# Optimization experiments

Hardware: AMD Instinct MI355X
Metric: run time of the kernel (lower is better)

Reference implementation:

```python
import jax, jax.numpy as jnp
import numpy as np

N_NODES = 50000
N_GRAPHS = 2048
BN_EPS = 1e-5


def setup_inputs() -> dict:
    key = jax.random.key(0)
    ks = jax.random.split(key, 12)
    n_feat, dim, n_out, n_edges = 128, 128, 12, 800000
    x = jax.random.normal(ks[0], (N_NODES, n_feat), dtype=jnp.float32)
    edge_index = jax.random.randint(ks[1], (2, n_edges), 0, N_NODES, dtype=jnp.int32)
    batch = jnp.sort(jax.random.randint(ks[2], (N_NODES,), 0, N_GRAPHS, dtype=jnp.int32))
    def lin(k, fan_in, fan_out):
        bound = 1.0 / np.sqrt(fan_in)
        kw, kb = jax.random.split(k)
        W = jax.random.uniform(kw, (fan_in, fan_out), minval=-bound, maxval=bound, dtype=jnp.float32)
        b = jax.random.uniform(kb, (fan_out,), minval=-bound, maxval=bound, dtype=jnp.float32)
        return W, b
    W1, b1 = lin(ks[3], n_feat, dim)
    W2, b2 = lin(ks[4], dim, dim)
    gamma = jnp.ones((dim,), dtype=jnp.float32)
    beta = jnp.zeros((dim,), dtype=jnp.float32)
    Wf1, bf1 = lin(ks[5], dim, 2 * dim)
    Wf2, bf2 = lin(ks[6], 2 * dim, n_out)
    return {"x": x, "edge_index": edge_index, "batch": batch,
            "W1": W1, "b1": b1, "W2": W2, "b2": b2,
            "gamma": gamma, "beta": beta,
            "Wf1": Wf1, "bf1": bf1, "Wf2": Wf2, "bf2": bf2}


def reference(x, edge_index, batch, W1, b1, W2, b2, gamma, beta, Wf1, bf1, Wf2, bf2):
    src, dst = edge_index[0], edge_index[1]
    # GINConv (eps=0): h = nn1(x + sum_{j in N(i)} x_j), scatter-add at dst
    agg = jax.ops.segment_sum(x[src], dst, num_segments=N_NODES)  # [N, F]
    h = x + agg
    h = jax.nn.relu(h @ W1 + b1) @ W2 + b2  # nn1 MLP
    h = jax.nn.relu(h)
    # BatchNorm1d (training mode: batch statistics, biased variance)
    mean = jnp.mean(h, axis=0)
    var = jnp.mean((h - mean) ** 2, axis=0)
    h = (h - mean) * jax.lax.rsqrt(var + BN_EPS) * gamma + beta
    # global_add_pool over graphs
    g = jax.ops.segment_sum(h, batch, num_segments=N_GRAPHS)  # [G, dim]
    g = jax.nn.relu(g @ Wf1 + bf1)
    return g @ Wf2 + bf2  # [G, n_outputs]
```

## Files before the change

### kernel.cpp

```cpp
#include <hip/hip_runtime.h>

#define N_FEAT   128
#define N_GRAPHS 2048
#define BN_EPS   1e-5f
#define LDA      136
#define FHLD     132
#define EPB      2048

typedef __attribute__((ext_vector_type(8))) short  bf16x8;
typedef __attribute__((ext_vector_type(4))) float  f32x4;

__device__ __forceinline__ unsigned short f2bf(float f) {
    union { float f; unsigned int u; } c; c.f = f;
    unsigned int r = c.u + 0x7fffu + ((c.u >> 16) & 1u);
    return (unsigned short)(r >> 16);
}
__device__ __forceinline__ float bf2f(unsigned short h) {
    union { unsigned int u; float f; } c; c.u = ((unsigned int)h) << 16;
    return c.f;
}

__device__ __forceinline__ void acc8(float* a, int4 u) {
    unsigned int w[4] = {(unsigned int)u.x, (unsigned int)u.y,
                         (unsigned int)u.z, (unsigned int)u.w};
    #pragma unroll
    for (int k = 0; k < 4; ++k) {
        a[2 * k]     += __uint_as_float(w[k] << 16);
        a[2 * k + 1] += __uint_as_float(w[k] & 0xffff0000u);
    }
}

__global__ __launch_bounds__(256) void k_cvtx(const float* __restrict__ x,
                                              unsigned short* __restrict__ xb,
                                              int n8)
{
    int i = blockIdx.x * 256 + threadIdx.x;
    if (i >= n8) return;
    float4 a = ((const float4*)x)[i * 2];
    float4 b = ((const float4*)x)[i * 2 + 1];
    ushort4 u0, u1;
    u0.x = f2bf(a.x); u0.y = f2bf(a.y); u0.z = f2bf(a.z); u0.w = f2bf(a.w);
    u1.x = f2bf(b.x); u1.y = f2bf(b.y); u1.z = f2bf(b.z); u1.w = f2bf(b.w);
    ((ushort4*)xb)[i * 2]     = u0;
    ((ushort4*)xb)[i * 2 + 1] = u1;
}

__global__ __launch_bounds__(256) void k_ghist(const int* __restrict__ batch,
                                               int* __restrict__ cnt, int n)
{
    int i = blockIdx.x * 256 + threadIdx.x;
    if (i < n) atomicAdd(&cnt[batch[i]], 1);
}

__global__ __launch_bounds__(256) void k_bhist(const int* __restrict__ dst,
                                               int* __restrict__ bcnt,
                                               int n_edges, int nb2)
{
    __shared__ int lc[256];
    int t = threadIdx.x;
    lc[t] = 0;
    __syncthreads();
    int base = blockIdx.x * EPB;
    for (int i = t; i < EPB; i += 256) {
        int e = base + i;
        if (e < n_edges) atomicAdd(&lc[dst[e] >> 8], 1);
    }
    __syncthreads();
    bcnt[t * nb2 + blockIdx.x] = lc[t];
}

__global__ __launch_bounds__(256) void k_bsum(const int* __restrict__ v,
                                              int* __restrict__ chsum, int n)
{
    __shared__ int s[256];
    int t = threadIdx.x;
    int i = blockIdx.x * 256 + t;
    s[t] = (i < n) ? v[i] : 0;
    __syncthreads();
    for (int o = 128; o > 0; o >>= 1) {
        if (t < o) s[t] += s[t + o];
        __syncthreads();
    }
    if (t == 0) chsum[blockIdx.x] = s[0];
}

__global__ __launch_bounds__(1024) void k_bscan2(const int* __restrict__ chsum,
                                                 int* __restrict__ choff, int nchunk)
{
    __shared__ int s[1024];
    int t = threadIdx.x;
    int v = (t < nchunk) ? chsum[t] : 0;
    s[t] = v;
    __syncthreads();
    for (int o = 1; o < 1024; o <<= 1) {
        int u = (t >= o) ? s[t - o] : 0;
        __syncthreads();
        s[t] += u;
        __syncthreads();
    }
    choff[t] = s[t] - v;
}

__global__ __launch_bounds__(256) void k_bapply(const int* __restrict__ v,
                                                const int* __restrict__ choff,
                                                int* __restrict__ out, int n)
{
    __shared__ int s[256];
    int t = threadIdx.x;
    int i = blockIdx.x * 256 + t;
    int c = (i < n) ? v[i] : 0;
    s[t] = c;
    __syncthreads();
    for (int o = 1; o < 256; o <<= 1) {
        int u = (t >= o) ? s[t - o] : 0;
        __syncthreads();
        s[t] += u;
        __syncthreads();
    }
    if (i < n) out[i] = choff[blockIdx.x] + s[t] - c;
}

__global__ __launch_bounds__(256) void k_part(const int* __restrict__ src,
                                              const int* __restrict__ dst,
                                              const int* __restrict__ boff2,
                                              unsigned* __restrict__ epart,
                                              int n_edges, int nb2)
{
    __shared__ int lc[256];
    __shared__ int lofs[256];
    __shared__ unsigned buf[EPB];
    int t = threadIdx.x, blk = blockIdx.x;
    int base = blk * EPB;
    lc[t] = 0;
    __syncthreads();
    for (int i = t; i < EPB; i += 256) {
        int e = base + i;
        if (e < n_edges) atomicAdd(&lc[dst[e] >> 8], 1);
    }
    __syncthreads();
    int v = lc[t];
    lofs[t] = v;
    __syncthreads();
    for (int o = 1; o < 256; o <<= 1) {
        int u = (t >= o) ? lofs[t - o] : 0;
        __syncthreads();
        lofs[t] += u;
        __syncthreads();
    }
    int excl = lofs[t] - v;
    __syncthreads();
    lofs[t] = excl;
    lc[t] = 0;
    __syncthreads();
    for (int i = t; i < EPB; i += 256) {
        int e = base + i;
        if (e < n_edges) {
            int d = dst[e];
            int b = d >> 8;
            unsigned pack = ((unsigned)d << 16) | (unsigned)src[e];
            int r = atomicAdd(&lc[b], 1);
            buf[lofs[b] + r] = pack;
        }
    }
    __syncthreads();
    int total = min(EPB, n_edges - base);
    for (int i = t; i < total; i += 256) {
        unsigned pack = buf[i];
        int b = pack >> 24;
        int gpos = boff2[b * nb2 + blk] + (i - lofs[b]);
        epart[gpos] = pack;
    }
}

__global__ __launch_bounds__(256) void k_bfill(const unsigned* __restrict__ epart,
                                               const int* __restrict__ boff2,
                                               int* __restrict__ row_start,
                                               unsigned short* __restrict__ csr,
                                               int n_nodes, int nb2, int nbkt)
{
    __shared__ int cur[256];
    __shared__ int sc2[256];
    __shared__ unsigned short seg[8192];
    int t = threadIdx.x, b = blockIdx.x;
    int node0 = b * 256;
    int nodes = min(256, n_nodes - node0);
    int ebeg = boff2[(size_t)b * nb2];
    int eend = (b + 1 < nbkt) ? boff2[(size_t)(b + 1) * nb2] : boff2[(size_t)nbkt * nb2];

    cur[t] = 0;
    __syncthreads();
    for (int i = ebeg + t; i < eend; i += 256)
        atomicAdd(&cur[(epart[i] >> 16) - node0], 1);
    __syncthreads();
    int v = cur[t];
    sc2[t] = v;
    __syncthreads();
    for (int o = 1; o < 256; o <<= 1) {
        int u = (t >= o) ? sc2[t - o] : 0;
        __syncthreads();
        sc2[t] += u;
        __syncthreads();
    }
    int excl = sc2[t] - v;
    if (t < nodes) row_start[node0 + t] = ebeg + excl;
    if (b == nbkt - 1 && t == 0) row_start[n_nodes] = eend;
    __syncthreads();
    cur[t] = excl;
    __syncthreads();
    for (int i = ebeg + t; i < eend; i += 256) {
        unsigned pack = epart[i];
        int idx = (pack >> 16) - node0;
        int slot = atomicAdd(&cur[idx], 1);
        seg[slot] = (unsigned short)(pack & 0xffffu);
    }
    __syncthreads();
    int seglen = eend - ebeg;
    for (int i = t; i < seglen; i += 256) csr[ebeg + i] = seg[i];
}

__global__ __launch_bounds__(256) void k_gather(const float* __restrict__ x,
                                                const unsigned short* __restrict__ xb,
                                                const unsigned short* __restrict__ csr,
                                                const int* __restrict__ row_start,
                                                unsigned short* __restrict__ Ahi,
                                                unsigned short* __restrict__ Alo,
                                                int n_nodes)
{
    int node = blockIdx.x * 4 + (threadIdx.x >> 6);
    if (node >= n_nodes) return;
    int l = threadIdx.x & 63;
    int q = l >> 4;
    int lq = l & 15;
    const int4* xb4 = (const int4*)xb;
    int beg = row_start[node], end = row_start[node + 1];
    float a[8];
    #pragma unroll
    for (int i = 0; i < 8; ++i) a[i] = 0.f;

    int j = beg + q;
    for (; j + 4 < end; j += 8) {
        int s0 = csr[j], s1 = csr[j + 4];
        int4 u0 = xb4[(size_t)s0 * 16 + lq];
        int4 u1 = xb4[(size_t)s1 * 16 + lq];
        acc8(a, u0);
        acc8(a, u1);
    }
    for (; j < end; j += 4) {
        int4 u = xb4[(size_t)csr[j] * 16 + lq];
        acc8(a, u);
    }
    #pragma unroll
    for (int i = 0; i < 8; ++i) {
        a[i] += __shfl_xor(a[i], 16);
        a[i] += __shfl_xor(a[i], 32);
    }
    if (q == 0) {
        float4 s0 = ((const float4*)(x + (size_t)node * 128))[lq * 2];
        float4 s1 = ((const float4*)(x + (size_t)node * 128))[lq * 2 + 1];
        a[0] += s0.x; a[1] += s0.y; a[2] += s0.z; a[3] += s0.w;
        a[4] += s1.x; a[5] += s1.y; a[6] += s1.z; a[7] += s1.w;
        unsigned int hw[4], lw[4];
        #pragma unroll
        for (int i = 0; i < 4; ++i) {
            unsigned short h0 = f2bf(a[2 * i]);
            unsigned short h1 = f2bf(a[2 * i + 1]);
            unsigned short l0 = f2bf(a[2 * i] - bf2f(h0));
            unsigned short l1 = f2bf(a[2 * i + 1] - bf2f(h1));
            hw[i] = (unsigned int)h0 | ((unsigned int)h1 << 16);
            lw[i] = (unsigned int)l0 | ((unsigned int)l1 << 16);
        }
        int4 hv = make_int4(hw[0], hw[1], hw[2], hw[3]);
        int4 lv = make_int4(lw[0], lw[1], lw[2], lw[3]);
        *(int4*)(Ahi + (size_t)node * 128 + lq * 8) = hv;
        *(int4*)(Alo + (size_t)node * 128 + lq * 8) = lv;
    }
}

__global__ __launch_bounds__(256) void k_mlp1_mfma(const unsigned short* __restrict__ Ahi,
                                                   const unsigned short* __restrict__ Alo,
                                                   const unsigned short* __restrict__ Wt1,
                                                   const float* __restrict__ b1,
                                                   const unsigned short* __restrict__ Wt2,
                                                   const float* __restrict__ b2,
                                                   const int* __restrict__ batch,
                                                   float* __restrict__ g_raw,
                                                   float* __restrict__ partial,
                                                   int n_rows)
{
    __shared__ __align__(16) char smem[64 * LDA * 2 * sizeof(unsigned short)];
    unsigned short* sHi = (unsigned short*)smem;
    unsigned short* sLo = sHi + 64 * LDA;

    int t = threadIdx.x;
    int wave = t >> 6, l = t & 63;
    int lr = l & 15;
    int lk = l >> 4;
    int row0 = blockIdx.x * 64;
    int col0 = wave * 32;

    #pragma unroll
    for (int it = 0; it < 4; ++it) {
        int idx = it * 256 + t;
        int r = idx >> 4, c8 = idx & 15;
        int gr = row0 + r;
        int4 vh = make_int4(0, 0, 0, 0), vl = make_int4(0, 0, 0, 0);
        if (gr < n_rows) {
            vh = ((const int4*)(Ahi + (size_t)gr * 128))[c8];
            vl = ((const int4*)(Alo + (size_t)gr * 128))[c8];
        }
        *(int4*)&sHi[r * LDA + c8 * 8] = vh;
        *(int4*)&sLo[r * LDA + c8 * 8] = vl;
    }
    __syncthreads();

    f32x4 acc[4][2];
    #pragma unroll
    for (int m = 0; m < 4; ++m)
        #pragma unroll
        for (int n = 0; n < 2; ++n) acc[m][n] = (f32x4){0.f, 0.f, 0.f, 0.f};

    #pragma unroll
    for (int ks = 0; ks < 4; ++ks) {
        bf16x8 bfrag[2];
        #pragma unroll
        for (int n = 0; n < 2; ++n) {
            int c = col0 + n * 16 + lr;
            bfrag[n] = *(const bf16x8*)(Wt1 + (size_t)c * 128 + ks * 32 + lk * 8);
        }
        #pragma unroll
        for (int m = 0; m < 4; ++m) {
            bf16x8 ah = *(const bf16x8*)&sHi[(m * 16 + lr) * LDA + ks * 32 + lk * 8];
            bf16x8 al = *(const bf16x8*)&sLo[(m * 16 + lr) * LDA + ks * 32 + lk * 8];
            #pragma unroll
            for (int n = 0; n < 2; ++n) {
                acc[m][n] = __builtin_amdgcn_mfma_f32_16x16x32_bf16(ah, bfrag[n], acc[m][n], 0, 0, 0);
                acc[m][n] = __builtin_amdgcn_mfma_f32_16x16x32_bf16(al, bfrag[n], acc[m][n], 0, 0, 0);
            }
        }
    }
    __syncthreads();

    #pragma unroll
    for (int n = 0; n < 2; ++n) {
        int c = col0 + n * 16 + lr;
        float bb = b1[c];
        #pragma unroll
        for (int m = 0; m < 4; ++m) {
            #pragma unroll
            for (int i = 0; i < 4; ++i) {
                int r = m * 16 + lk * 4 + i;
                float v = fmaxf(acc[m][n][i] + bb, 0.f);
                unsigned short hb = f2bf(v);
                sHi[r * LDA + c] = hb;
                sLo[r * LDA + c] = f2bf(v - bf2f(hb));
            }
        }
    }
    __syncthreads();

    #pragma unroll
    for (int m = 0; m < 4; ++m)
        #pragma unroll
        for (int n = 0; n < 2; ++n) acc[m][n] = (f32x4){0.f, 0.f, 0.f, 0.f};

    #pragma unroll
    for (int ks = 0; ks < 4; ++ks) {
        bf16x8 bfrag[2];
        #pragma unroll
        for (int n = 0; n < 2; ++n) {
            int c = col0 + n * 16 + lr;
            bfrag[n] = *(const bf16x8*)(Wt2 + (size_t)c * 128 + ks * 32 + lk * 8);
        }
        #pragma unroll
        for (int m = 0; m < 4; ++m) {
            bf16x8 ah = *(const bf16x8*)&sHi[(m * 16 + lr) * LDA + ks * 32 + lk * 8];
            bf16x8 al = *(const bf16x8*)&sLo[(m * 16 + lr) * LDA + ks * 32 + lk * 8];
            #pragma unroll
            for (int n = 0; n < 2; ++n) {
                acc[m][n] = __builtin_amdgcn_mfma_f32_16x16x32_bf16(ah, bfrag[n], acc[m][n], 0, 0, 0);
                acc[m][n] = __builtin_amdgcn_mfma_f32_16x16x32_bf16(al, bfrag[n], acc[m][n], 0, 0, 0);
            }
        }
    }

    float bb0 = b2[col0 + lr];
    float bb1 = b2[col0 + 16 + lr];
    int c0 = col0 + lr, c1 = col0 + 16 + lr;
    float v0s[4][4], v1s[4][4];
    float ps[2] = {0.f, 0.f}, pq[2] = {0.f, 0.f};
    #pragma unroll
    for (int m = 0; m < 4; ++m) {
        #pragma unroll
        for (int i = 0; i < 4; ++i) {
            int gr = row0 + m * 16 + lk * 4 + i;
            float v0 = fmaxf(acc[m][0][i] + bb0, 0.f);
            float v1 = fmaxf(acc[m][1][i] + bb1, 0.f);
            if (gr >= n_rows) { v0 = 0.f; v1 = 0.f; }
            v0s[m][i] = v0; v1s[m][i] = v1;
            ps[0] += v0; pq[0] += v0 * v0;
            ps[1] += v1; pq[1] += v1 * v1;
        }
    }
    #pragma unroll
    for (int n = 0; n < 2; ++n) {
        ps[n] += __shfl_xor(ps[n], 16); ps[n] += __shfl_xor(ps[n], 32);
        pq[n] += __shfl_xor(pq[n], 16); pq[n] += __shfl_xor(pq[n], 32);
    }
    if (lk == 0) {
        partial[(size_t)blockIdx.x * 256 + c0]       = ps[0];
        partial[(size_t)blockIdx.x * 256 + c1]       = ps[1];
        partial[(size_t)blockIdx.x * 256 + 128 + c0] = pq[0];
        partial[(size_t)blockIdx.x * 256 + 128 + c1] = pq[1];
    }

    __syncthreads();
    float (*fH)[FHLD] = (float (*)[FHLD])smem;
    int* sB = (int*)(smem + 64 * FHLD * sizeof(float));
    if (t < 64) sB[t] = (row0 + t < n_rows) ? batch[row0 + t] : -1;
    #pragma unroll
    for (int m = 0; m < 4; ++m) {
        #pragma unroll
        for (int i = 0; i < 4; ++i) {
            int r = m * 16 + lk * 4 + i;
            fH[r][c0] = v0s[m][i];
            fH[r][c1] = v1s[m][i];
        }
    }
    __syncthreads();

    {
        int c = t & 127;
        int rbeg = (t >> 7) * 32, rend = rbeg + 32;
        float a = 0.f;
        int bcur = sB[rbeg];
        for (int r = rbeg; r < rend; ++r) {
            int b = sB[r];
            if (b != bcur) {
                if (bcur >= 0) unsafeAtomicAdd(&g_raw[(size_t)bcur * 128 + c], a);
                a = 0.f; bcur = b;
            }
            a += fH[r][c];
        }
        if (bcur >= 0) unsafeAtomicAdd(&g_raw[(size_t)bcur * 128 + c], a);
    }
}

__global__ __launch_bounds__(256) void k_cvtW(const float* __restrict__ W1,
                                              const float* __restrict__ W2,
                                              unsigned short* __restrict__ Wt1,
                                              unsigned short* __restrict__ Wt2)
{
    int i = blockIdx.x * 256 + threadIdx.x;
    int which = i >> 14;
    int k = (i >> 7) & 127;
    int c = i & 127;
    const float* W = which ? W2 : W1;
    unsigned short* O = which ? Wt2 : Wt1;
    O[c * 128 + k] = f2bf(W[k * 128 + c]);
}

__global__ __launch_bounds__(256) void k_bnred(const float* __restrict__ partial,
                                               float* __restrict__ stats, int nblk)
{
    int j = threadIdx.x;
    float s = 0.f;
    for (int b = blockIdx.x; b < nblk; b += gridDim.x)
        s += partial[(size_t)b * 256 + j];
    unsafeAtomicAdd(&stats[j], s);
}

__global__ void k_bnfin(const float* __restrict__ stats,
                        const float* __restrict__ gamma,
                        const float* __restrict__ beta,
                        float* __restrict__ sc, int n_rows)
{
    int f = threadIdx.x;
    float inv_n = 1.0f / (float)n_rows;
    float mean = stats[f] * inv_n;
    float var = stats[128 + f] * inv_n - mean * mean;
    float inv = rsqrtf(var + BN_EPS);
    float scale = gamma[f] * inv;
    sc[f] = scale;
    sc[128 + f] = beta[f] - mean * scale;
}

__global__ __launch_bounds__(256) void k_head(const float* __restrict__ g_raw,
                                              const int* __restrict__ cnt,
                                              const float* __restrict__ sc,
                                              const float* __restrict__ Wf1,
                                              const float* __restrict__ bf1,
                                              const float* __restrict__ Wf2,
                                              const float* __restrict__ bf2,
                                              float* __restrict__ out)
{
    __shared__ float sg[128];
    __shared__ float sh[256];
    int t = threadIdx.x;
    int G = blockIdx.x;
    if (t < 128) {
        float c = (float)cnt[G];
        sg[t] = g_raw[(size_t)G * 128 + t] * sc[t] + c * sc[128 + t];
    }
    __syncthreads();
    float a = bf1[t];
    #pragma unroll 8
    for (int k = 0; k < 128; ++k) a = fmaf(sg[k], Wf1[k * 256 + t], a);
    sh[t] = fmaxf(a, 0.f);
    __syncthreads();
    if (t < 192) {
        int o = t >> 4, l = t & 15;
        float p = 0.f;
        for (int k = l; k < 256; k += 16) p += sh[k] * Wf2[k * 12 + o];
        #pragma unroll
        for (int m = 8; m >= 1; m >>= 1) p += __shfl_xor(p, m, 16);
        if (l == 0) out[(size_t)G * 12 + o] = p + bf2[o];
    }
}

extern "C" void kernel_launch(void* const* d_in, const int* in_sizes, int n_in,
                              void* d_out, int out_size, void* d_ws, size_t ws_size,
                              hipStream_t stream)
{
    const float* x     = (const float*)d_in[0];
    const int*   ei    = (const int*)d_in[1];
    const int*   batch = (const int*)d_in[2];
    const float* W1    = (const float*)d_in[3];
    const float* b1    = (const float*)d_in[4];
    const float* W2    = (const float*)d_in[5];
    const float* b2    = (const float*)d_in[6];
    const float* gamma = (const float*)d_in[7];
    const float* beta  = (const float*)d_in[8];
    const float* Wf1   = (const float*)d_in[9];
    const float* bf1   = (const float*)d_in[10];
    const float* Wf2   = (const float*)d_in[11];
    const float* bf2   = (const float*)d_in[12];

    int n_nodes = in_sizes[0] / N_FEAT;
    int n_edges = in_sizes[1] / 2;
    const int* src = ei;
    const int* dst = ei + n_edges;

    char* ws = (char*)d_ws;
    size_t planeBytes = (size_t)n_nodes * N_FEAT * sizeof(unsigned short);
    size_t gBytes     = (size_t)N_GRAPHS * N_FEAT * sizeof(float);
    int nblk_m = (n_nodes + 63) / 64;
    int nb2    = (n_edges + EPB - 1) / EPB;
    int nbkt   = (n_nodes + 255) / 256;
    int nscan  = 256 * nb2;
    int nchunk = (nscan + 255) / 256;

    unsigned short* Ahi = (unsigned short*)ws;
    unsigned short* Alo = (unsigned short*)(ws + planeBytes);
    unsigned short* xb  = (unsigned short*)(ws + 2 * planeBytes);
    float* g_raw = (float*)(ws + 3 * planeBytes);
    float* stats = (float*)((char*)g_raw + gBytes);
    float* sc    = stats + 256;
    int*   cnt   = (int*)(sc + 256);
    unsigned short* Wt1 = (unsigned short*)(cnt + N_GRAPHS);
    unsigned short* Wt2 = Wt1 + 128 * 128;
    float* partial = (float*)(Wt2 + 128 * 128);
    char* p = (char*)(partial + (size_t)nblk_m * 256);
    int* row_start = (int*)p;   p += (size_t)(n_nodes + 1) * sizeof(int);
    int* bcnt      = (int*)p;   p += (size_t)nscan * sizeof(int);
    int* bch       = (int*)p;   p += 1024 * sizeof(int);
    int* bchoff    = (int*)p;   p += 1024 * sizeof(int);
    int* boff2     = (int*)p;   p += (size_t)nscan * sizeof(int);
    unsigned* epart = (unsigned*)p;  p += (size_t)n_edges * sizeof(unsigned);
    unsigned short* csr = (unsigned short*)p;

    hipMemsetAsync(g_raw, 0, gBytes + (256 + 256 + N_GRAPHS) * sizeof(float), stream);

    int n8 = n_nodes * N_FEAT / 8;
    k_cvtx<<<(n8 + 255) / 256, 256, 0, stream>>>(x, xb, n8);
    k_cvtW<<<128, 256, 0, stream>>>(W1, W2, Wt1, Wt2);
    k_ghist<<<(n_nodes + 255) / 256, 256, 0, stream>>>(batch, cnt, n_nodes);

    k_bhist<<<nb2, 256, 0, stream>>>(dst, bcnt, n_edges, nb2);
    k_bsum<<<nchunk, 256, 0, stream>>>(bcnt, bch, nscan);
    k_bscan2<<<1, 1024, 0, stream>>>(bch, bchoff, nchunk);
    k_bapply<<<nchunk, 256, 0, stream>>>(bcnt, bchoff, boff2, nscan);
    k_part<<<nb2, 256, 0, stream>>>(src, dst, boff2, epart, n_edges, nb2);
    k_bfill<<<nbkt, 256, 0, stream>>>(epart, boff2, row_start, csr, n_nodes, nb2, nbkt);

    k_gather<<<(n_nodes + 3) / 4, 256, 0, stream>>>(x, xb, csr, row_start, Ahi, Alo, n_nodes);

    k_mlp1_mfma<<<nblk_m, 256, 0, stream>>>(Ahi, Alo, Wt1, b1, Wt2, b2, batch,
                                            g_raw, partial, n_nodes);

    k_bnred<<<64, 256, 0, stream>>>(partial, stats, nblk_m);
    k_bnfin<<<1, 128, 0, stream>>>(stats, gamma, beta, sc, n_nodes);
    k_head<<<N_GRAPHS, 256, 0, stream>>>(g_raw, cnt, sc, Wf1, bf1, Wf2, bf2, (float*)d_out);
}
```

Before: 134.1 us.

## Fuse neighbor gather into MFMA MLP kernel and merge prep kernels

The CSR neighbor aggregation now runs inside the MLP GEMM kernel, writing the hi/lo bf16 split straight into shared memory. This removes the Ahi/Alo global round trip and one launch. Separately, the x conversion, weight transpose and graph histogram kernels are merged into one launch with block-range dispatch. The catch is that gather parallelism drops: each wave handles 16 nodes in sequence, with only 782 blocks of 256 threads, so latency hiding for the random gathers may suffer.

```diff
diff --git a/kernel.cpp b/kernel.cpp
--- a/kernel.cpp
+++ b/kernel.cpp
@@ -30,26 +30,39 @@
     }
 }
 
-__global__ __launch_bounds__(256) void k_cvtx(const float* __restrict__ x,
+__global__ __launch_bounds__(256) void k_prep(const float* __restrict__ x,
                                               unsigned short* __restrict__ xb,
-                                              int n8)
-{
-    int i = blockIdx.x * 256 + threadIdx.x;
-    if (i >= n8) return;
-    float4 a = ((const float4*)x)[i * 2];
-    float4 b = ((const float4*)x)[i * 2 + 1];
-    ushort4 u0, u1;
-    u0.x = f2bf(a.x); u0.y = f2bf(a.y); u0.z = f2bf(a.z); u0.w = f2bf(a.w);
-    u1.x = f2bf(b.x); u1.y = f2bf(b.y); u1.z = f2bf(b.z); u1.w = f2bf(b.w);
-    ((ushort4*)xb)[i * 2]     = u0;
-    ((ushort4*)xb)[i * 2 + 1] = u1;
-}
-
-__global__ __launch_bounds__(256) void k_ghist(const int* __restrict__ batch,
-                                               int* __restrict__ cnt, int n)
-{
-    int i = blockIdx.x * 256 + threadIdx.x;
-    if (i < n) atomicAdd(&cnt[batch[i]], 1);
+                                              int n8, int nbx,
+                                              const float* __restrict__ W1,
+                                              const float* __restrict__ W2,
+                                              unsigned short* __restrict__ Wt1,
+                                              unsigned short* __restrict__ Wt2,
+                                              const int* __restrict__ batch,
+                                              int* __restrict__ cnt, int n_nodes)
+{
+    int b = blockIdx.x, t = threadIdx.x;
+    if (b < nbx) {
+        int i = b * 256 + t;
+        if (i >= n8) return;
+        float4 a = ((const float4*)x)[i * 2];
+        float4 c = ((const float4*)x)[i * 2 + 1];
+        ushort4 u0, u1;
+        u0.x = f2bf(a.x); u0.y = f2bf(a.y); u0.z = f2bf(a.z); u0.w = f2bf(a.w);
+        u1.x = f2bf(c.x); u1.y = f2bf(c.y); u1.z = f2bf(c.z); u1.w = f2bf(c.w);
+        ((ushort4*)xb)[i * 2]     = u0;
+        ((ushort4*)xb)[i * 2 + 1] = u1;
+    } else if (b < nbx + 128) {
+        int i = (b - nbx) * 256 + t;
+        int which = i >> 14;
+        int k = (i >> 7) & 127;
+        int c = i & 127;
+        const float* W = which ? W2 : W1;
+        unsigned short* O = which ? Wt2 : Wt1;
+        O[c * 128 + k] = f2bf(W[k * 128 + c]);
+    } else {
+        int i = (b - nbx - 128) * 256 + t;
+        if (i < n_nodes) atomicAdd(&cnt[batch[i]], 1);
+    }
 }
 
 __global__ __launch_bounds__(256) void k_bhist(const int* __restrict__ dst,
@@ -218,74 +231,18 @@
     for (int i = t; i < seglen; i += 256) csr[ebeg + i] = seg[i];
 }
 
-__global__ __launch_bounds__(256) void k_gather(const float* __restrict__ x,
-                                                const unsigned short* __restrict__ xb,
-                                                const unsigned short* __restrict__ csr,
-                                                const int* __restrict__ row_start,
-                                                unsigned short* __restrict__ Ahi,
-                                                unsigned short* __restrict__ Alo,
-                                                int n_nodes)
-{
-    int node = blockIdx.x * 4 + (threadIdx.x >> 6);
-    if (node >= n_nodes) return;
-    int l = threadIdx.x & 63;
-    int q = l >> 4;
-    int lq = l & 15;
-    const int4* xb4 = (const int4*)xb;
-    int beg = row_start[node], end = row_start[node + 1];
-    float a[8];
-    #pragma unroll
-    for (int i = 0; i < 8; ++i) a[i] = 0.f;
-
-    int j = beg + q;
-    for (; j + 4 < end; j += 8) {
-        int s0 = csr[j], s1 = csr[j + 4];
-        int4 u0 = xb4[(size_t)s0 * 16 + lq];
-        int4 u1 = xb4[(size_t)s1 * 16 + lq];
-        acc8(a, u0);
-        acc8(a, u1);
-    }
-    for (; j < end; j += 4) {
-        int4 u = xb4[(size_t)csr[j] * 16 + lq];
-        acc8(a, u);
-    }
-    #pragma unroll
-    for (int i = 0; i < 8; ++i) {
-        a[i] += __shfl_xor(a[i], 16);
-        a[i] += __shfl_xor(a[i], 32);
-    }
-    if (q == 0) {
-        float4 s0 = ((const float4*)(x + (size_t)node * 128))[lq * 2];
-        float4 s1 = ((const float4*)(x + (size_t)node * 128))[lq * 2 + 1];
-        a[0] += s0.x; a[1] += s0.y; a[2] += s0.z; a[3] += s0.w;
-        a[4] += s1.x; a[5] += s1.y; a[6] += s1.z; a[7] += s1.w;
-        unsigned int hw[4], lw[4];
-        #pragma unroll
-        for (int i = 0; i < 4; ++i) {
-            unsigned short h0 = f2bf(a[2 * i]);
-            unsigned short h1 = f2bf(a[2 * i + 1]);
-            unsigned short l0 = f2bf(a[2 * i] - bf2f(h0));
-            unsigned short l1 = f2bf(a[2 * i + 1] - bf2f(h1));
-            hw[i] = (unsigned int)h0 | ((unsigned int)h1 << 16);
-            lw[i] = (unsigned int)l0 | ((unsigned int)l1 << 16);
-        }
-        int4 hv = make_int4(hw[0], hw[1], hw[2], hw[3]);
-        int4 lv = make_int4(lw[0], lw[1], lw[2], lw[3]);
-        *(int4*)(Ahi + (size_t)node * 128 + lq * 8) = hv;
-        *(int4*)(Alo + (size_t)node * 128 + lq * 8) = lv;
-    }
-}
-
-__global__ __launch_bounds__(256) void k_mlp1_mfma(const unsigned short* __restrict__ Ahi,
-                                                   const unsigned short* __restrict__ Alo,
-                                                   const unsigned short* __restrict__ Wt1,
-                                                   const float* __restrict__ b1,
-                                                   const unsigned short* __restrict__ Wt2,
-                                                   const float* __restrict__ b2,
-                                                   const int* __restrict__ batch,
-                                                   float* __restrict__ g_raw,
-                                                   float* __restrict__ partial,
-                                                   int n_rows)
+__global__ __launch_bounds__(256) void k_gemm(const float* __restrict__ x,
+                                              const unsigned short* __restrict__ xb,
+                                              const unsigned short* __restrict__ csr,
+                                              const int* __restrict__ row_start,
+                                              const unsigned short* __restrict__ Wt1,
+                                              const float* __restrict__ b1,
+                                              const unsigned short* __restrict__ Wt2,
+                                              const float* __restrict__ b2,
+                                              const int* __restrict__ batch,
+                                              float* __restrict__ g_raw,
+                                              float* __restrict__ partial,
+                                              int n_rows)
 {
     __shared__ __align__(16) char smem[64 * LDA * 2 * sizeof(unsigned short)];
     unsigned short* sHi = (unsigned short*)smem;
@@ -298,18 +255,53 @@
     int row0 = blockIdx.x * 64;
     int col0 = wave * 32;
 
-    #pragma unroll
-    for (int it = 0; it < 4; ++it) {
-        int idx = it * 256 + t;
-        int r = idx >> 4, c8 = idx & 15;
-        int gr = row0 + r;
-        int4 vh = make_int4(0, 0, 0, 0), vl = make_int4(0, 0, 0, 0);
-        if (gr < n_rows) {
-            vh = ((const int4*)(Ahi + (size_t)gr * 128))[c8];
-            vl = ((const int4*)(Alo + (size_t)gr * 128))[c8];
-        }
-        *(int4*)&sHi[r * LDA + c8 * 8] = vh;
-        *(int4*)&sLo[r * LDA + c8 * 8] = vl;
+    const int4* xb4 = (const int4*)xb;
+    for (int i = 0; i < 16; ++i) {
+        int r = wave * 16 + i;
+        int node = row0 + r;
+        float a[8];
+        #pragma unroll
+        for (int k = 0; k < 8; ++k) a[k] = 0.f;
+        if (node < n_rows) {
+            int beg = row_start[node], end = row_start[node + 1];
+            int j = beg + lk;
+            for (; j + 4 < end; j += 8) {
+                int s0 = csr[j], s1 = csr[j + 4];
+                int4 u0 = xb4[(size_t)s0 * 16 + lr];
+                int4 u1 = xb4[(size_t)s1 * 16 + lr];
+                acc8(a, u0);
+                acc8(a, u1);
+            }
+            for (; j < end; j += 4) {
+                int4 u = xb4[(size_t)csr[j] * 16 + lr];
+                acc8(a, u);
+            }
+        }
+        #pragma unroll
+        for (int k = 0; k < 8; ++k) {
+            a[k] += __shfl_xor(a[k], 16);
+            a[k] += __shfl_xor(a[k], 32);
+        }
+        if (lk == 0) {
+            if (node < n_rows) {
+                float4 s0 = ((const float4*)(x + (size_t)node * 128))[lr * 2];
+                float4 s1 = ((const float4*)(x + (size_t)node * 128))[lr * 2 + 1];
+                a[0] += s0.x; a[1] += s0.y; a[2] += s0.z; a[3] += s0.w;
+                a[4] += s1.x; a[5] += s1.y; a[6] += s1.z; a[7] += s1.w;
+            }
+            unsigned int hw[4], lw[4];
+            #pragma unroll
+            for (int k = 0; k < 4; ++k) {
+                unsigned short h0 = f2bf(a[2 * k]);
+                unsigned short h1 = f2bf(a[2 * k + 1]);
+                unsigned short l0 = f2bf(a[2 * k] - bf2f(h0));
+                unsigned short l1 = f2bf(a[2 * k + 1] - bf2f(h1));
+                hw[k] = (unsigned int)h0 | ((unsigned int)h1 << 16);
+                lw[k] = (unsigned int)l0 | ((unsigned int)l1 << 16);
+            }
+            *(int4*)&sHi[r * LDA + lr * 8] = make_int4(hw[0], hw[1], hw[2], hw[3]);
+            *(int4*)&sLo[r * LDA + lr * 8] = make_int4(lw[0], lw[1], lw[2], lw[3]);
+        }
     }
     __syncthreads();
 
@@ -443,20 +435,6 @@
         }
         if (bcur >= 0) unsafeAtomicAdd(&g_raw[(size_t)bcur * 128 + c], a);
     }
-}
-
-__global__ __launch_bounds__(256) void k_cvtW(const float* __restrict__ W1,
-                                              const float* __restrict__ W2,
-                                              unsigned short* __restrict__ Wt1,
-                                              unsigned short* __restrict__ Wt2)
-{
-    int i = blockIdx.x * 256 + threadIdx.x;
-    int which = i >> 14;
-    int k = (i >> 7) & 127;
-    int c = i & 127;
-    const float* W = which ? W2 : W1;
-    unsigned short* O = which ? Wt2 : Wt1;
-    O[c * 128 + k] = f2bf(W[k * 128 + c]);
 }
 
 __global__ __launch_bounds__(256) void k_bnred(const float* __restrict__ partial,
@@ -549,10 +527,8 @@
     int nscan  = 256 * nb2;
     int nchunk = (nscan + 255) / 256;
 
-    unsigned short* Ahi = (unsigned short*)ws;
-    unsigned short* Alo = (unsigned short*)(ws + planeBytes);
-    unsigned short* xb  = (unsigned short*)(ws + 2 * planeBytes);
-    float* g_raw = (float*)(ws + 3 * planeBytes);
+    unsigned short* xb  = (unsigned short*)ws;
+    float* g_raw = (float*)(ws + planeBytes);
     float* stats = (float*)((char*)g_raw + gBytes);
     float* sc    = stats + 256;
     int*   cnt   = (int*)(sc + 256);
@@ -571,9 +547,10 @@
     hipMemsetAsync(g_raw, 0, gBytes + (256 + 256 + N_GRAPHS) * sizeof(float), stream);
 
     int n8 = n_nodes * N_FEAT / 8;
-    k_cvtx<<<(n8 + 255) / 256, 256, 0, stream>>>(x, xb, n8);
-    k_cvtW<<<128, 256, 0, stream>>>(W1, W2, Wt1, Wt2);
-    k_ghist<<<(n_nodes + 255) / 256, 256, 0, stream>>>(batch, cnt, n_nodes);
+    int nbx = (n8 + 255) / 256;
+    int nbg = (n_nodes + 255) / 256;
+    k_prep<<<nbx + 128 + nbg, 256, 0, stream>>>(x, xb, n8, nbx, W1, W2, Wt1, Wt2,
+                                                batch, cnt, n_nodes);
 
     k_bhist<<<nb2, 256, 0, stream>>>(dst, bcnt, n_edges, nb2);
     k_bsum<<<nchunk, 256, 0, stream>>>(bcnt, bch, nscan);
@@ -582,10 +559,8 @@
     k_part<<<nb2, 256, 0, stream>>>(src, dst, boff2, epart, n_edges, nb2);
     k_bfill<<<nbkt, 256, 0, stream>>>(epart, boff2, row_start, csr, n_nodes, nb2, nbkt);
 
-    k_gather<<<(n_nodes + 3) / 4, 256, 0, stream>>>(x, xb, csr, row_start, Ahi, Alo, n_nodes);
-
-    k_mlp1_mfma<<<nblk_m, 256, 0, stream>>>(Ahi, Alo, Wt1, b1, Wt2, b2, batch,
-                                            g_raw, partial, n_nodes);
+    k_gemm<<<nblk_m, 256, 0, stream>>>(x, xb, csr, row_start, Wt1, b1, Wt2, b2,
+                                       batch, g_raw, partial, n_nodes);
 
     k_bnred<<<64, 256, 0, stream>>>(partial, stats, nblk_m);
     k_bnfin<<<1, 128, 0, stream>>>(stats, gamma, beta, sc, n_nodes);
```

Result: slower. 146.5 us (+9.2%).
